# Kernel optimization log

Measured on AMD Instinct MI355X. Metric: run time of the kernel, lower is better.

The kernel has to match this reference:

```python
import jax
import jax.numpy as jnp
from jax import lax
import numpy as np

Y_SIZE = 64
X_SIZE = 50000
T_LEN = 1_000_000


def setup_inputs() -> dict:
    key = jax.random.key(0)
    kx, kt, kb, kp = jax.random.split(key, 4)
    x = jax.random.randint(kx, (T_LEN,), 0, X_SIZE, dtype=jnp.int32)
    transition = jax.random.uniform(kt, (Y_SIZE, Y_SIZE), dtype=jnp.float32)
    transition = transition / jnp.sum(transition, axis=1, keepdims=True)
    b = jax.random.uniform(kb, (Y_SIZE, X_SIZE), dtype=jnp.float32)
    b = b / jnp.sum(b, axis=1, keepdims=True)
    pi = jax.random.uniform(kp, (Y_SIZE,), dtype=jnp.float32)
    pi = pi / jnp.sum(pi)
    return {"x": x, "transition": transition, "b": b, "pi": pi}


def reference(x, transition, b, pi):
    """HMM.alpha_scaling: scaled forward recurrence.

    alpha[0]   = normalize(b[:, x[0]] * pi)
    alpha[t]   = normalize((alpha[t-1] @ transition) * b[:, x[t]])
    Returns the full (T, y_size) matrix of normalized forward probabilities,
    matching the torch loop (every stored row ends up sum-normalized).
    """
    a0 = b[:, x[0]] * pi                      # (y,)
    a0 = a0 / jnp.sum(a0)
    emis = b[:, x[1:]].T                      # (T-1, y) gathered emission probs

    def step(carry, e):
        new = (carry @ transition) * e        # (y,)
        new = new / jnp.sum(new)              # per-step scaling
        return new, new

    _, rest = lax.scan(step, a0, emis)        # rest: (T-1, y)
    return jnp.concatenate([a0[None, :], rest], axis=0)  # (T, y)
```

## Files before the change

### kernel.cpp

```cpp
#include <hip/hip_runtime.h>

#define TLEN 1000000
#define YS 64
#define XS 50000
#define CHUNK 32
#define WARM 16
#define SPAN (CHUNK + WARM)
#define NCHUNK ((TLEN + CHUNK - 1) / CHUNK)
#define RPW 16
#define NW ((NCHUNK + RPW - 1) / RPW)
#define WPB 4
#define NBLK ((NW + WPB - 1) / WPB)
#define BSCALE ((float)XS)

typedef float f32x4 __attribute__((ext_vector_type(4)));
typedef short bf16x8 __attribute__((ext_vector_type(8)));
typedef unsigned int u32x4 __attribute__((ext_vector_type(4)));
typedef unsigned int u32x2 __attribute__((ext_vector_type(2)));
typedef int i32x4 __attribute__((ext_vector_type(4)));

__device__ __forceinline__ unsigned cvtpk(float lo, float hi) {
  unsigned r;
  asm("v_cvt_pk_bf16_f32 %0, %1, %2" : "=v"(r) : "v"(lo), "v"(hi));
  return r;
}
__device__ __forceinline__ unsigned short f2bf_rne(float f) {
  unsigned u = __float_as_uint(f);
  unsigned r = (u + 0x7FFFu + ((u >> 16) & 1u)) >> 16;
  return (unsigned short)r;
}
__device__ __forceinline__ float bf2f(unsigned short u) {
  return __uint_as_float(((unsigned)u) << 16);
}
__device__ __forceinline__ float bfu_lo(unsigned d) { return __uint_as_float(d << 16); }
__device__ __forceinline__ float bfu_hi(unsigned d) { return __uint_as_float(d & 0xffff0000u); }
__device__ __forceinline__ int clamp01(int t) {
  t = t < 0 ? 0 : t;
  return t > (TLEN - 1) ? (TLEN - 1) : t;
}
__device__ __forceinline__ int clampB(int t) {
  t = t < 0 ? 0 : t;
  return t > (TLEN - 4) ? (TLEN - 4) : t;
}

template <bool USE_BT>
__global__ __launch_bounds__(256, 2) void hmm_fwd(
    const int* __restrict__ x, const float* __restrict__ A,
    const float* __restrict__ pi, const float* __restrict__ bsrc,
    const unsigned* __restrict__ bpk, float* __restrict__ out)
{
  __shared__ __align__(16) float wlds[WPB][16][68];
  const int wslot = threadIdx.x >> 6;
  const int wv = blockIdx.x * WPB + wslot;
  const int lane = threadIdx.x & 63;
  if (wv >= NW) return;
  const int g = lane >> 4, c15 = lane & 15;
  const int rr = lane >> 2, qq = lane & 3;
  float (*wrow)[68] = wlds[wslot];

  bf16x8 Bhi[2][4], Blo[2][4];
#pragma unroll
  for (int h = 0; h < 2; h++)
#pragma unroll
    for (int nt = 0; nt < 4; nt++) {
      bf16x8 bh, bl;
#pragma unroll
      for (int j = 0; j < 8; j++) {
        int k = 32 * h + g * 8 + j;
        int c = 16 * nt + c15;
        float av = A[k * YS + c];
        unsigned short hb = f2bf_rne(av);
        bh[j] = (short)hb;
        bl[j] = (short)f2bf_rne(av - bf2f(hb));
      }
      Bhi[h][nt] = bh; Blo[h][nt] = bl;
    }

  const int c0 = wv * RPW;

  int trow = (c0 + rr) * CHUNK - WARM;

#pragma unroll
  for (int j = 0; j < 4; j++)
#pragma unroll
    for (int nt = 0; nt < 4; nt++)
      wrow[g * 4 + j][16 * nt + c15] = 1.0f;

  float o[4];
  {
    int x0v = x[0];
#pragma unroll
    for (int nt = 0; nt < 4; nt++) {
      int c = 16 * nt + c15;
      o[nt] = pi[c] * bsrc[(size_t)c * XS + x0v] * BSCALE;
    }
  }
  const bool isw0 = (wv == 0);

  auto eload2 = [&](int xt, unsigned& d0, unsigned& d1) {
    if (USE_BT) {
      u32x2 d = *(const u32x2*)(bpk + (size_t)(unsigned)xt * 32 + 2 * c15);
      d0 = d.x; d1 = d.y;
    } else {
      float e0 = bsrc[(size_t)(c15 +  0) * XS + xt] * BSCALE;
      float e1 = bsrc[(size_t)(c15 + 16) * XS + xt] * BSCALE;
      float e2 = bsrc[(size_t)(c15 + 32) * XS + xt] * BSCALE;
      float e3 = bsrc[(size_t)(c15 + 48) * XS + xt] * BSCALE;
      d0 = cvtpk(e0, e1); d1 = cvtpk(e2, e3);
    }
  };

  unsigned er[4][4][2];
  i32x4 xq[4], xqn[4];
  int bj[4];
#pragma unroll
  for (int j = 0; j < 4; j++) {
    int tj0 = (c0 + 4 * g + j) * CHUNK - WARM;
#pragma unroll
    for (int u = 0; u < 4; u++)
      eload2(x[clamp01(tj0 + u)], er[u][j][0], er[u][j][1]);
    bj[j] = tj0 + 4;
    xq[j] = *(const i32x4*)(x + clampB(bj[j]));
  }

  const f32x4 z4 = {0.f, 0.f, 0.f, 0.f};

  auto stepf = [&](int sabs, int u) {
    const f32x4* wr = (const f32x4*)&wrow[c15][0];
    f32x4 q0 = wr[2 * g];
    f32x4 q1 = wr[2 * g + 1];
    f32x4 q2 = wr[2 * g + 8];
    f32x4 q3 = wr[2 * g + 9];
    union { u32x4 u4; bf16x8 b; } ua0, ua1;
    ua0.u4 = (u32x4){cvtpk(q0.x, q0.y), cvtpk(q0.z, q0.w), cvtpk(q1.x, q1.y), cvtpk(q1.z, q1.w)};
    ua1.u4 = (u32x4){cvtpk(q2.x, q2.y), cvtpk(q2.z, q2.w), cvtpk(q3.x, q3.y), cvtpk(q3.z, q3.w)};
    bf16x8 a0 = ua0.b, a1 = ua1.b;

    f32x4 C[4];
#pragma unroll
    for (int nt = 0; nt < 4; nt++) {
      f32x4 c = __builtin_amdgcn_mfma_f32_16x16x32_bf16(a0, Bhi[0][nt], z4, 0, 0, 0);
      c = __builtin_amdgcn_mfma_f32_16x16x32_bf16(a0, Blo[0][nt], c, 0, 0, 0);
      c = __builtin_amdgcn_mfma_f32_16x16x32_bf16(a1, Bhi[1][nt], c, 0, 0, 0);
      c = __builtin_amdgcn_mfma_f32_16x16x32_bf16(a1, Blo[1][nt], c, 0, 0, 0);
      C[nt] = c;
    }

    float w[4][4];
#pragma unroll
    for (int j = 0; j < 4; j++) {
      unsigned d0 = er[u][j][0], d1 = er[u][j][1];
      w[0][j] = C[0][j] * bfu_lo(d0);
      w[1][j] = C[1][j] * bfu_hi(d0);
      w[2][j] = C[2][j] * bfu_lo(d1);
      w[3][j] = C[3][j] * bfu_hi(d1);
    }

    if (isw0 && sabs <= WARM) {
#pragma unroll
      for (int nt = 0; nt < 4; nt++)
        w[nt][0] = (lane < 16) ? o[nt] : w[nt][0];
    }

#pragma unroll
    for (int j = 0; j < 4; j++)
#pragma unroll
      for (int nt = 0; nt < 4; nt++)
        wrow[g * 4 + j][16 * nt + c15] = w[nt][j];

#pragma unroll
    for (int j = 0; j < 4; j++) {
      eload2(xq[j][u], er[u][j][0], er[u][j][1]);
      if (u == 0) xqn[j] = *(const i32x4*)(x + clampB(bj[j] + 4));
    }

    if (sabs >= WARM) {
      f32x4 v0 = *(const f32x4*)&wrow[rr][ 0 + 4 * qq];
      f32x4 v1 = *(const f32x4*)&wrow[rr][16 + 4 * qq];
      f32x4 v2 = *(const f32x4*)&wrow[rr][32 + 4 * qq];
      f32x4 v3 = *(const f32x4*)&wrow[rr][48 + 4 * qq];
      f32x4 vs = (v0 + v1) + (v2 + v3);
      float s = (vs.x + vs.y) + (vs.z + vs.w);
      s += __shfl_xor(s, 1);
      s += __shfl_xor(s, 2);
      float rs = __builtin_amdgcn_rcpf(s);
      if (trow < TLEN) {
        float* po = out + (size_t)trow * YS + 4 * qq;
        *(f32x4*)(po +  0) = v0 * rs;
        *(f32x4*)(po + 16) = v1 * rs;
        *(f32x4*)(po + 32) = v2 * rs;
        *(f32x4*)(po + 48) = v3 * rs;
      }
    }
    trow += 1;
  };

  for (int s = 0; s < SPAN; s += 4) {
    stepf(s + 0, 0);
    stepf(s + 1, 1);
    stepf(s + 2, 2);
    stepf(s + 3, 3);
#pragma unroll
    for (int j = 0; j < 4; j++) {
      xq[j] = xqn[j];
      bj[j] += 4;
    }
  }
}

__global__ __launch_bounds__(256) void pack_b(
    const float* __restrict__ b, unsigned* __restrict__ bpk)
{
  __shared__ float tile[64][65];
  int x0 = blockIdx.x << 6;
  int lane = threadIdx.x & 63;
  int w = threadIdx.x >> 6;
  int xg = x0 + lane;
#pragma unroll
  for (int yy = 0; yy < 64; yy += 4) {
    int y = yy + w;
    tile[y][lane] = (xg < XS) ? b[(size_t)y * XS + xg] * BSCALE : 0.f;
  }
  __syncthreads();
  int s2 = threadIdx.x & 31;
  int xo = threadIdx.x >> 5;
  int c15 = s2 >> 1, p = s2 & 1;
  int colA = c15 + 32 * p, colB = colA + 16;
#pragma unroll
  for (int pass = 0; pass < 8; pass++) {
    int xl = pass * 8 + xo;
    int xcur = x0 + xl;
    if (xcur < XS)
      bpk[(size_t)xcur * 32 + s2] = cvtpk(tile[colA][xl], tile[colB][xl]);
  }
}

extern "C" void kernel_launch(void* const* d_in, const int* in_sizes, int n_in,
                              void* d_out, int out_size, void* d_ws, size_t ws_size,
                              hipStream_t stream)
{
  const int*   x  = (const int*)d_in[0];
  const float* A  = (const float*)d_in[1];
  const float* b  = (const float*)d_in[2];
  const float* pi = (const float*)d_in[3];
  float* out = (float*)d_out;

  const size_t bpk_bytes = (size_t)XS * 32 * sizeof(unsigned);

  if (ws_size >= bpk_bytes) {
    unsigned* bpk = (unsigned*)d_ws;
    int tblocks = (XS + 63) / 64;
    pack_b<<<tblocks, 256, 0, stream>>>(b, bpk);
    hmm_fwd<true><<<NBLK, 256, 0, stream>>>(x, A, pi, b, bpk, out);
  } else {
    hmm_fwd<false><<<NBLK, 256, 0, stream>>>(x, A, pi, b, nullptr, out);
  }
}
```

Before: 88.36 us.

## Halve chunk length, drop bf16 lo-split of transition, raise occupancy

Chunks shrink from 32 to 16 rows, so each wave's serial run drops from 48 steps to 32. There are twice as many waves, with launch bounds raised to 4 blocks per CU. The transition matrix now uses only its bf16 high part, which halves the MFMAs per step at the cost of accuracy. Emission prefetch depth is cut from 4 to 2, the reciprocal gets a Newton refinement, and output pointers are incremented directly. The catch is more total warm-up work relative to useful output, plus lower precision in the matrix-vector product.

New measurement: 91.42 us. +3.5%, slower.

```diff
diff --git a/kernel.cpp b/kernel.cpp
--- a/kernel.cpp
+++ b/kernel.cpp
@@ -3,7 +3,7 @@
 #define TLEN 1000000
 #define YS 64
 #define XS 50000
-#define CHUNK 32
+#define CHUNK 16
 #define WARM 16
 #define SPAN (CHUNK + WARM)
 #define NCHUNK ((TLEN + CHUNK - 1) / CHUNK)
@@ -17,7 +17,6 @@
 typedef short bf16x8 __attribute__((ext_vector_type(8)));
 typedef unsigned int u32x4 __attribute__((ext_vector_type(4)));
 typedef unsigned int u32x2 __attribute__((ext_vector_type(2)));
-typedef int i32x4 __attribute__((ext_vector_type(4)));
 
 __device__ __forceinline__ unsigned cvtpk(float lo, float hi) {
   unsigned r;
@@ -28,9 +27,6 @@
   unsigned u = __float_as_uint(f);
   unsigned r = (u + 0x7FFFu + ((u >> 16) & 1u)) >> 16;
   return (unsigned short)r;
-}
-__device__ __forceinline__ float bf2f(unsigned short u) {
-  return __uint_as_float(((unsigned)u) << 16);
 }
 __device__ __forceinline__ float bfu_lo(unsigned d) { return __uint_as_float(d << 16); }
 __device__ __forceinline__ float bfu_hi(unsigned d) { return __uint_as_float(d & 0xffff0000u); }
@@ -38,13 +34,9 @@
   t = t < 0 ? 0 : t;
   return t > (TLEN - 1) ? (TLEN - 1) : t;
 }
-__device__ __forceinline__ int clampB(int t) {
-  t = t < 0 ? 0 : t;
-  return t > (TLEN - 4) ? (TLEN - 4) : t;
-}
 
 template <bool USE_BT>
-__global__ __launch_bounds__(256, 2) void hmm_fwd(
+__global__ __launch_bounds__(256, 4) void hmm_fwd(
     const int* __restrict__ x, const float* __restrict__ A,
     const float* __restrict__ pi, const float* __restrict__ bsrc,
     const unsigned* __restrict__ bpk, float* __restrict__ out)
@@ -58,27 +50,26 @@
   const int rr = lane >> 2, qq = lane & 3;
   float (*wrow)[68] = wlds[wslot];
 
-  bf16x8 Bhi[2][4], Blo[2][4];
+  bf16x8 Bf[2][4];
 #pragma unroll
   for (int h = 0; h < 2; h++)
 #pragma unroll
     for (int nt = 0; nt < 4; nt++) {
-      bf16x8 bh, bl;
+      bf16x8 bh;
 #pragma unroll
       for (int j = 0; j < 8; j++) {
         int k = 32 * h + g * 8 + j;
         int c = 16 * nt + c15;
-        float av = A[k * YS + c];
-        unsigned short hb = f2bf_rne(av);
-        bh[j] = (short)hb;
-        bl[j] = (short)f2bf_rne(av - bf2f(hb));
+        bh[j] = (short)f2bf_rne(A[k * YS + c]);
       }
-      Bhi[h][nt] = bh; Blo[h][nt] = bl;
+      Bf[h][nt] = bh;
     }
 
   const int c0 = wv * RPW;
 
   int trow = (c0 + rr) * CHUNK - WARM;
+  float* pout = out + (size_t)(trow < 0 ? 0 : trow) * YS + 4 * qq;
+  pout = out + (long)trow * YS + 4 * qq;
 
 #pragma unroll
   for (int j = 0; j < 4; j++)
@@ -110,22 +101,21 @@
     }
   };
 
-  unsigned er[4][4][2];
-  i32x4 xq[4], xqn[4];
-  int bj[4];
+  int tj0[4];
+  unsigned er[2][4][2];
+  int xs[2][4];
 #pragma unroll
   for (int j = 0; j < 4; j++) {
-    int tj0 = (c0 + 4 * g + j) * CHUNK - WARM;
-#pragma unroll
-    for (int u = 0; u < 4; u++)
-      eload2(x[clamp01(tj0 + u)], er[u][j][0], er[u][j][1]);
-    bj[j] = tj0 + 4;
-    xq[j] = *(const i32x4*)(x + clampB(bj[j]));
+    tj0[j] = (c0 + 4 * g + j) * CHUNK - WARM;
+    eload2(x[clamp01(tj0[j] + 0)], er[0][j][0], er[0][j][1]);
+    eload2(x[clamp01(tj0[j] + 1)], er[1][j][0], er[1][j][1]);
+    xs[0][j] = x[clamp01(tj0[j] + 2)];
+    xs[1][j] = x[clamp01(tj0[j] + 3)];
   }
 
   const f32x4 z4 = {0.f, 0.f, 0.f, 0.f};
 
-  auto stepf = [&](int sabs, int u) {
+  auto stepf = [&](int sabs, int ue) {
     const f32x4* wr = (const f32x4*)&wrow[c15][0];
     f32x4 q0 = wr[2 * g];
     f32x4 q1 = wr[2 * g + 1];
@@ -139,39 +129,36 @@
     f32x4 C[4];
 #pragma unroll
     for (int nt = 0; nt < 4; nt++) {
-      f32x4 c = __builtin_amdgcn_mfma_f32_16x16x32_bf16(a0, Bhi[0][nt], z4, 0, 0, 0);
-      c = __builtin_amdgcn_mfma_f32_16x16x32_bf16(a0, Blo[0][nt], c, 0, 0, 0);
-      c = __builtin_amdgcn_mfma_f32_16x16x32_bf16(a1, Bhi[1][nt], c, 0, 0, 0);
-      c = __builtin_amdgcn_mfma_f32_16x16x32_bf16(a1, Blo[1][nt], c, 0, 0, 0);
+      f32x4 c = __builtin_amdgcn_mfma_f32_16x16x32_bf16(a0, Bf[0][nt], z4, 0, 0, 0);
+      c = __builtin_amdgcn_mfma_f32_16x16x32_bf16(a1, Bf[1][nt], c, 0, 0, 0);
       C[nt] = c;
     }
 
-    float w[4][4];
 #pragma unroll
     for (int j = 0; j < 4; j++) {
-      unsigned d0 = er[u][j][0], d1 = er[u][j][1];
-      w[0][j] = C[0][j] * bfu_lo(d0);
-      w[1][j] = C[1][j] * bfu_hi(d0);
-      w[2][j] = C[2][j] * bfu_lo(d1);
-      w[3][j] = C[3][j] * bfu_hi(d1);
+      unsigned d0 = er[ue][j][0], d1 = er[ue][j][1];
+      C[0][j] *= bfu_lo(d0);
+      C[1][j] *= bfu_hi(d0);
+      C[2][j] *= bfu_lo(d1);
+      C[3][j] *= bfu_hi(d1);
     }
 
     if (isw0 && sabs <= WARM) {
 #pragma unroll
       for (int nt = 0; nt < 4; nt++)
-        w[nt][0] = (lane < 16) ? o[nt] : w[nt][0];
+        C[nt][0] = (lane < 16) ? o[nt] : C[nt][0];
     }
 
 #pragma unroll
     for (int j = 0; j < 4; j++)
 #pragma unroll
       for (int nt = 0; nt < 4; nt++)
-        wrow[g * 4 + j][16 * nt + c15] = w[nt][j];
+        wrow[g * 4 + j][16 * nt + c15] = C[nt][j];
 
 #pragma unroll
     for (int j = 0; j < 4; j++) {
-      eload2(xq[j][u], er[u][j][0], er[u][j][1]);
-      if (u == 0) xqn[j] = *(const i32x4*)(x + clampB(bj[j] + 4));
+      eload2(xs[ue][j], er[ue][j][0], er[ue][j][1]);
+      xs[ue][j] = x[clamp01(tj0[j] + sabs + 4)];
     }
 
     if (sabs >= WARM) {
@@ -183,28 +170,22 @@
       float s = (vs.x + vs.y) + (vs.z + vs.w);
       s += __shfl_xor(s, 1);
       s += __shfl_xor(s, 2);
-      float rs = __builtin_amdgcn_rcpf(s);
+      float r0 = __builtin_amdgcn_rcpf(s);
+      float rs = r0 * fmaf(-s, r0, 2.0f);
       if (trow < TLEN) {
-        float* po = out + (size_t)trow * YS + 4 * qq;
-        *(f32x4*)(po +  0) = v0 * rs;
-        *(f32x4*)(po + 16) = v1 * rs;
-        *(f32x4*)(po + 32) = v2 * rs;
-        *(f32x4*)(po + 48) = v3 * rs;
+        *(f32x4*)(pout +  0) = v0 * rs;
+        *(f32x4*)(pout + 16) = v1 * rs;
+        *(f32x4*)(pout + 32) = v2 * rs;
+        *(f32x4*)(pout + 48) = v3 * rs;
       }
     }
     trow += 1;
+    pout += YS;
   };
 
-  for (int s = 0; s < SPAN; s += 4) {
+  for (int s = 0; s < SPAN; s += 2) {
     stepf(s + 0, 0);
     stepf(s + 1, 1);
-    stepf(s + 2, 2);
-    stepf(s + 3, 3);
-#pragma unroll
-    for (int j = 0; j < 4; j++) {
-      xq[j] = xqn[j];
-      bj[j] += 4;
-    }
   }
 }
 
```
